# Kernel optimization log

Hardware: AMD Instinct MI355X
Metric: run time of the kernel (lower is better)

The kernel has to match this reference:

```python
import jax, jax.numpy as jnp
import numpy as np

B, TQ, TK, D, DV = 16, 2048, 2048, 128, 128
MASK_VAL = -1000000.0

def setup_inputs() -> dict:
    key = jax.random.key(0)
    kq, kk, kv, kl = jax.random.split(key, 4)
    q = jax.random.normal(kq, (B, TQ, D), dtype=jnp.float32)
    k = jax.random.normal(kk, (B, TK, D), dtype=jnp.float32)
    v = jax.random.normal(kv, (B, TK, DV), dtype=jnp.float32)
    valid_lens = jax.random.randint(kl, (B,), 1, TK, dtype=jnp.int64)
    return {"q": q, "k": k, "v": v, "valid_lens": valid_lens}

def reference(q, k, v, valid_lens):
    d = q.shape[-1]
    # scores: [B, Tq, Tk]
    scores = jnp.einsum('bqd,bkd->bqk', q, k) / jnp.sqrt(jnp.asarray(d, q.dtype))
    # mask key positions >= valid_len (same per-batch length for every query row)
    mask = jnp.arange(scores.shape[-1])[None, None, :] < valid_lens[:, None, None]
    scores = jnp.where(mask, scores, jnp.asarray(MASK_VAL, scores.dtype))
    attn = jax.nn.softmax(scores, axis=-1)
    # dropout p=0.0 (eval mode) -> identity
    return jnp.einsum('bqk,bkv->bqv', attn, v)
```

## Files before the change

kernel.cpp:

```cpp
#include <hip/hip_runtime.h>
#include <math.h>

#define NB 16
#define TQ 2048
#define TK 2048
#define DD 128
#define DVV 128

constexpr int QTILE = 64;
constexpr int KTILE = 32;
#define PSTR 40

typedef __attribute__((ext_vector_type(8))) _Float16 half8;
typedef __attribute__((ext_vector_type(4))) _Float16 half4;
typedef __attribute__((ext_vector_type(4))) float f32x4;

__device__ inline float fast_exp2(float x) {
#if __has_builtin(__builtin_amdgcn_exp2f)
    return __builtin_amdgcn_exp2f(x);
#else
    return exp2f(x);
#endif
}
__device__ inline void setprio1() { __builtin_amdgcn_s_setprio(1); }
__device__ inline void setprio0() { __builtin_amdgcn_s_setprio(0); }

__device__ inline void glds16(const _Float16* g, _Float16* l) {
    __builtin_amdgcn_global_load_lds(
        (const __attribute__((address_space(1))) void*)g,
        (__attribute__((address_space(3))) void*)l, 16, 0, 0);
}

__global__ __launch_bounds__(256)
void repack(const float* __restrict__ kg, const float* __restrict__ vg,
            const int* __restrict__ vlg,
            _Float16* __restrict__ Kpk, _Float16* __restrict__ Vpk)
{
    const int bt = blockIdx.x;
    const int b = bt >> 6, t = bt & 63;
    if (t * KTILE >= vlg[b]) return;
    const int tid = threadIdx.x;

    __shared__ float Vlds[32][129];

    const float* kin = kg + ((size_t)b * TK + t * KTILE) * DD;
    _Float16* kout = Kpk + ((size_t)bt << 12);
#pragma unroll
    for (int pp = 0; pp < 2; ++pp) {
        int s = tid + pp * 256;
        int ct = s >> 8, c = (s >> 6) & 3, ln = s & 63;
        int kr = ct * 16 + (ln & 15), kc = c * 32 + ((ln >> 4) & 3) * 8;
        const float* ip = kin + kr * DD + kc;
        float4 f0 = *(const float4*)ip;
        float4 f1 = *(const float4*)(ip + 4);
        half8 h;
        h[0] = (_Float16)f0.x; h[1] = (_Float16)f0.y;
        h[2] = (_Float16)f0.z; h[3] = (_Float16)f0.w;
        h[4] = (_Float16)f1.x; h[5] = (_Float16)f1.y;
        h[6] = (_Float16)f1.z; h[7] = (_Float16)f1.w;
        *(half8*)(kout + (size_t)s * 8) = h;
    }

    const float* vin = vg + ((size_t)b * TK + t * KTILE) * DVV;
#pragma unroll
    for (int pp = 0; pp < 4; ++pp) {
        int idx = tid + pp * 256;
        int r = idx >> 5, c4 = (idx & 31) * 4;
        float4 f = *(const float4*)(vin + r * DVV + c4);
        Vlds[r][c4 + 0] = f.x; Vlds[r][c4 + 1] = f.y;
        Vlds[r][c4 + 2] = f.z; Vlds[r][c4 + 3] = f.w;
    }
    __syncthreads();
    _Float16* vout = Vpk + ((size_t)bt << 12);
#pragma unroll
    for (int pp = 0; pp < 2; ++pp) {
        int s = tid + pp * 256;
        int n = s >> 6, ln = s & 63;
        int dv = n * 16 + (ln & 15), k0 = ((ln >> 4) & 3) * 8;
        half8 h;
#pragma unroll
        for (int j = 0; j < 8; ++j)
            h[j] = (_Float16)Vlds[k0 + j][dv];
        *(half8*)(vout + (size_t)s * 8) = h;
    }
}

__global__ __launch_bounds__(256, 4)
void attn_fwd(const float* __restrict__ qg,
              const _Float16* __restrict__ Kpk, const _Float16* __restrict__ Vpk,
              const int* __restrict__ vlg,
              float* __restrict__ outg, float* __restrict__ wso,
              float* __restrict__ wsml, int ns)
{
    __shared__ _Float16 Kb[2][4096];
    __shared__ _Float16 Vb[2][4096];
    __shared__ _Float16 Plds[4][16][PSTR];

    const int tid  = threadIdx.x;
    const int wid  = tid >> 6;
    const int lane = tid & 63;
    const int l15  = lane & 15;
    const int lhi  = lane >> 4;

    const int bid   = blockIdx.x;
    const int b     = bid & (NB - 1);
    const int qbase = (bid >> 4) * QTILE;
    const int sp    = blockIdx.y;

    const int VL  = vlg[b];
    const int nkt = (VL + KTILE - 1) / KTILE;
    const int tps = (nkt + ns - 1) / ns;
    const int t0  = sp * tps;
    const int t1  = min(nkt, t0 + tps);
    if (t0 >= t1) return;

    const _Float16* ktb = Kpk + ((size_t)(b * 64) << 12);
    const _Float16* vtb = Vpk + ((size_t)(b * 64) << 12);

    half8 qf[4];
    {
        const float scale = 0.08838834764831845f * 1.4426950408889634f;
        const int qrow = qbase + wid * 16 + l15;
        const float* qp = qg + (size_t)(b * TQ + qrow) * DD + lhi * 8;
#pragma unroll
        for (int c = 0; c < 4; ++c) {
            float4 f0 = *(const float4*)(qp + c * 32);
            float4 f1 = *(const float4*)(qp + c * 32 + 4);
            half8 t;
            t[0] = (_Float16)(f0.x * scale); t[1] = (_Float16)(f0.y * scale);
            t[2] = (_Float16)(f0.z * scale); t[3] = (_Float16)(f0.w * scale);
            t[4] = (_Float16)(f1.x * scale); t[5] = (_Float16)(f1.y * scale);
            t[6] = (_Float16)(f1.z * scale); t[7] = (_Float16)(f1.w * scale);
            qf[c] = t;
        }
    }

    auto STAGE = [&](int buf, int t) {
        const _Float16* kp = ktb + ((size_t)t << 12) + wid * 1024 + lane * 8;
        const _Float16* vp = vtb + ((size_t)t << 12) + wid * 1024 + lane * 8;
        glds16(kp,       &Kb[buf][wid * 1024]);
        glds16(kp + 512, &Kb[buf][wid * 1024 + 512]);
        glds16(vp,       &Vb[buf][wid * 1024]);
        glds16(vp + 512, &Vb[buf][wid * 1024 + 512]);
    };

    float m_i = -INFINITY, l_i = 0.f;
    f32x4 o[8];
#pragma unroll
    for (int n = 0; n < 8; ++n) { f32x4 z = {0.f, 0.f, 0.f, 0.f}; o[n] = z; }

    STAGE(0, t0);
    int cur = 0;
    for (int t = t0; t < t1; ++t) {
        const int kb = t * KTILE;
        const bool pre = (t + 1 < t1);
        if (pre) STAGE(cur ^ 1, t + 1);

        if (pre) asm volatile("s_waitcnt vmcnt(4)\ns_barrier" ::: "memory");
        else     asm volatile("s_waitcnt vmcnt(0)\ns_barrier" ::: "memory");

        const half8* kp = (const half8*)&Kb[cur][0];
        const half8* vp = (const half8*)&Vb[cur][0];

        f32x4 sc[2];
        setprio1();
#pragma unroll
        for (int ct = 0; ct < 2; ++ct) {
            f32x4 z = {0.f, 0.f, 0.f, 0.f};
            sc[ct] = z;
#pragma unroll
            for (int c = 0; c < 4; ++c) {
                half8 kf = kp[ct * 256 + c * 64 + lane];
                sc[ct] = __builtin_amdgcn_mfma_f32_16x16x32_f16(kf, qf[c], sc[ct], 0, 0, 0);
            }
        }
        setprio0();

        if (kb + KTILE > VL) {
#pragma unroll
            for (int ct = 0; ct < 2; ++ct) {
                const int kg = kb + ct * 16 + lhi * 4;
#pragma unroll
                for (int r = 0; r < 4; ++r)
                    if (kg + r >= VL) sc[ct][r] = -1e30f;
            }
        }

        float mx = sc[0][0];
#pragma unroll
        for (int ct = 0; ct < 2; ++ct)
#pragma unroll
            for (int r = 0; r < 4; ++r) mx = fmaxf(mx, sc[ct][r]);
        mx = fmaxf(mx, __shfl_xor(mx, 16));
        mx = fmaxf(mx, __shfl_xor(mx, 32));

        const bool skip = __all(mx <= m_i + 8.0f);
        const float mnew = skip ? m_i : fmaxf(m_i, mx);

        float p[8];
        float sum = 0.f;
#pragma unroll
        for (int ct = 0; ct < 2; ++ct)
#pragma unroll
            for (int r = 0; r < 4; ++r) {
                float e = fast_exp2(sc[ct][r] - mnew);
                p[ct * 4 + r] = e;
                sum += e;
            }
        sum += __shfl_xor(sum, 16);
        sum += __shfl_xor(sum, 32);

#pragma unroll
        for (int ct = 0; ct < 2; ++ct) {
            half4 ph;
            ph[0] = (_Float16)p[ct * 4 + 0]; ph[1] = (_Float16)p[ct * 4 + 1];
            ph[2] = (_Float16)p[ct * 4 + 2]; ph[3] = (_Float16)p[ct * 4 + 3];
            *(half4*)&Plds[wid][l15][ct * 16 + lhi * 4] = ph;
        }

        if (skip) {
            l_i += sum;
        } else {
            const float corr = fast_exp2(m_i - mnew);
            l_i = l_i * corr + sum;
            m_i = mnew;
            float cr[4];
#pragma unroll
            for (int r = 0; r < 4; ++r)
                cr[r] = __shfl(corr, (lane & 48) | (lhi * 4 + r));
#pragma unroll
            for (int n = 0; n < 8; ++n)
#pragma unroll
                for (int r = 0; r < 4; ++r) o[n][r] *= cr[r];
        }

        half8 pa = *(const half8*)&Plds[wid][l15][lhi * 8];
        setprio1();
#pragma unroll
        for (int n = 0; n < 8; ++n) {
            half8 vb = vp[n * 64 + lane];
            o[n] = __builtin_amdgcn_mfma_f32_16x16x32_f16(pa, vb, o[n], 0, 0, 0);
        }
        setprio0();

        asm volatile("s_waitcnt lgkmcnt(0)\ns_barrier" ::: "memory");
        cur ^= 1;
    }

    if (ns == 1) {
        float li4[4];
#pragma unroll
        for (int r = 0; r < 4; ++r) {
            float lr = __shfl(l_i, (lane & 48) | (lhi * 4 + r));
            li4[r] = 1.0f / lr;
        }
#pragma unroll
        for (int r = 0; r < 4; ++r) {
            const int qrow = qbase + wid * 16 + lhi * 4 + r;
            float* op = outg + (size_t)(b * TQ + qrow) * DVV + l15;
#pragma unroll
            for (int n = 0; n < 8; ++n)
                op[n * 16] = o[n][r] * li4[r];
        }
    } else {
        if (lhi == 0) {
            float2 ml = make_float2(m_i, l_i);
            *(float2*)&wsml[((size_t)(sp * NB + b) * TQ + qbase + wid * 16 + l15) * 2] = ml;
        }
        float* po = wso + ((size_t)(sp * NB + b) * TQ + qbase + wid * 16) * DVV;
#pragma unroll
        for (int r = 0; r < 4; ++r)
#pragma unroll
            for (int n = 0; n < 8; ++n)
                po[(lhi * 4 + r) * DVV + n * 16 + l15] = o[n][r];
    }
}

__global__ __launch_bounds__(256)
void attn_combine(const float* __restrict__ wso, const float* __restrict__ wsml,
                  const int* __restrict__ vlg, float* __restrict__ outg, int ns)
{
    const int idx = blockIdx.x * 256 + threadIdx.x;
    const int d4 = idx & 31;
    const int q  = (idx >> 5) & (TQ - 1);
    const int b  = idx >> 16;

    const int VL  = vlg[b];
    const int nkt = (VL + KTILE - 1) / KTILE;
    const int tps = (nkt + ns - 1) / ns;
    const int nv  = (nkt + tps - 1) / tps;

    float M = -1e30f, den = 0.f;
    f32x4 acc = {0.f, 0.f, 0.f, 0.f};
    for (int s = 0; s < nv; ++s) {
        const size_t row = (size_t)(s * NB + b) * TQ + q;
        float2 ml = *(const float2*)&wsml[row * 2];
        float Mn = fmaxf(M, ml.x);
        float c  = fast_exp2(M - Mn);
        float w  = fast_exp2(ml.x - Mn);
        f32x4 ov = *(const f32x4*)&wso[row * DVV + d4 * 4];
        acc = acc * c + ov * w;
        den = den * c + w * ml.y;
        M = Mn;
    }
    const float inv = 1.0f / den;
    f32x4 r = acc * inv;
    *(f32x4*)&outg[((size_t)b * TQ + q) * DVV + d4 * 4] = r;
}

extern "C" void kernel_launch(void* const* d_in, const int* in_sizes, int n_in,
                              void* d_out, int out_size, void* d_ws, size_t ws_size,
                              hipStream_t stream) {
    const float* q  = (const float*)d_in[0];
    const float* k  = (const float*)d_in[1];
    const float* v  = (const float*)d_in[2];
    const int*   vl = (const int*)d_in[3];
    float* out = (float*)d_out;

    const size_t pk_elems = (size_t)NB * 64 * 4096;
    const size_t pk_bytes = pk_elems * sizeof(_Float16);
    const size_t o_elems  = (size_t)NB * TQ * DVV;
    const size_t ml_elems = (size_t)NB * TQ * 2;
    const size_t per_split = (o_elems + ml_elems) * sizeof(float);

    int ns = (ws_size >= 2 * pk_bytes + 2 * per_split) ? 2 : 1;

    _Float16* Kpk = (_Float16*)d_ws;
    _Float16* Vpk = Kpk + pk_elems;
    float* wso  = (float*)(Vpk + pk_elems);
    float* wsml = wso + (size_t)ns * o_elems;

    hipLaunchKernelGGL(repack, dim3(NB * 64), dim3(256), 0, stream,
                       k, v, vl, Kpk, Vpk);

    dim3 grid(NB * (TQ / QTILE), ns);
    hipLaunchKernelGGL(attn_fwd, grid, dim3(256), 0, stream,
                       q, Kpk, Vpk, vl, out, wso, wsml, ns);

    if (ns > 1) {
        dim3 cgrid((NB * TQ * (DVV / 4)) / 256);
        hipLaunchKernelGGL(attn_combine, cgrid, dim3(256), 0, stream,
                           wso, wsml, vl, out, ns);
    }
}
```

Measured before the change: 73.04 us.

## Use 128-row Q tiles with 8 waves, fp16 split partials, and up to 4 splits

Doubles the query tile to 128 rows and the block to 512 threads (8 waves), so each staged K/V tile feeds twice as many queries. Each wave now issues half as many async loads, with waves 0-3 loading K and 4-7 loading V. Split-K partial outputs are stored in fp16 instead of fp32, which halves workspace traffic. The split count can rise to 4 when the workspace allows. The fp16 partials lose some accuracy, and more splits add combine work.

```diff
diff --git a/kernel.cpp b/kernel.cpp
--- a/kernel.cpp
+++ b/kernel.cpp
@@ -7,7 +7,7 @@
 #define DD 128
 #define DVV 128
 
-constexpr int QTILE = 64;
+constexpr int QTILE = 128;
 constexpr int KTILE = 32;
 #define PSTR 40
 
@@ -85,16 +85,16 @@
     }
 }
 
-__global__ __launch_bounds__(256, 4)
+__global__ __launch_bounds__(512, 6)
 void attn_fwd(const float* __restrict__ qg,
               const _Float16* __restrict__ Kpk, const _Float16* __restrict__ Vpk,
               const int* __restrict__ vlg,
-              float* __restrict__ outg, float* __restrict__ wso,
+              float* __restrict__ outg, _Float16* __restrict__ wso,
               float* __restrict__ wsml, int ns)
 {
     __shared__ _Float16 Kb[2][4096];
     __shared__ _Float16 Vb[2][4096];
-    __shared__ _Float16 Plds[4][16][PSTR];
+    __shared__ _Float16 Plds[8][16][PSTR];
 
     const int tid  = threadIdx.x;
     const int wid  = tid >> 6;
@@ -135,13 +135,13 @@
         }
     }
 
+    const int qtr = wid & 3;
     auto STAGE = [&](int buf, int t) {
-        const _Float16* kp = ktb + ((size_t)t << 12) + wid * 1024 + lane * 8;
-        const _Float16* vp = vtb + ((size_t)t << 12) + wid * 1024 + lane * 8;
-        glds16(kp,       &Kb[buf][wid * 1024]);
-        glds16(kp + 512, &Kb[buf][wid * 1024 + 512]);
-        glds16(vp,       &Vb[buf][wid * 1024]);
-        glds16(vp + 512, &Vb[buf][wid * 1024 + 512]);
+        const _Float16* src = ((wid < 4) ? ktb : vtb)
+                              + ((size_t)t << 12) + qtr * 1024 + lane * 8;
+        _Float16* dst = (wid < 4) ? &Kb[buf][qtr * 1024] : &Vb[buf][qtr * 1024];
+        glds16(src, dst);
+        glds16(src + 512, dst + 512);
     };
 
     float m_i = -INFINITY, l_i = 0.f;
@@ -156,7 +156,7 @@
         const bool pre = (t + 1 < t1);
         if (pre) STAGE(cur ^ 1, t + 1);
 
-        if (pre) asm volatile("s_waitcnt vmcnt(4)\ns_barrier" ::: "memory");
+        if (pre) asm volatile("s_waitcnt vmcnt(2)\ns_barrier" ::: "memory");
         else     asm volatile("s_waitcnt vmcnt(0)\ns_barrier" ::: "memory");
 
         const half8* kp = (const half8*)&Kb[cur][0];
@@ -267,23 +267,23 @@
             float2 ml = make_float2(m_i, l_i);
             *(float2*)&wsml[((size_t)(sp * NB + b) * TQ + qbase + wid * 16 + l15) * 2] = ml;
         }
-        float* po = wso + ((size_t)(sp * NB + b) * TQ + qbase + wid * 16) * DVV;
+        _Float16* po = wso + ((size_t)(sp * NB + b) * TQ + qbase + wid * 16) * DVV;
 #pragma unroll
         for (int r = 0; r < 4; ++r)
 #pragma unroll
             for (int n = 0; n < 8; ++n)
-                po[(lhi * 4 + r) * DVV + n * 16 + l15] = o[n][r];
+                po[(lhi * 4 + r) * DVV + n * 16 + l15] = (_Float16)o[n][r];
     }
 }
 
 __global__ __launch_bounds__(256)
-void attn_combine(const float* __restrict__ wso, const float* __restrict__ wsml,
+void attn_combine(const _Float16* __restrict__ wso, const float* __restrict__ wsml,
                   const int* __restrict__ vlg, float* __restrict__ outg, int ns)
 {
     const int idx = blockIdx.x * 256 + threadIdx.x;
-    const int d4 = idx & 31;
-    const int q  = (idx >> 5) & (TQ - 1);
-    const int b  = idx >> 16;
+    const int d8 = idx & 15;
+    const int q  = (idx >> 4) & (TQ - 1);
+    const int b  = idx >> 15;
 
     const int VL  = vlg[b];
     const int nkt = (VL + KTILE - 1) / KTILE;
@@ -291,21 +291,26 @@
     const int nv  = (nkt + tps - 1) / tps;
 
     float M = -1e30f, den = 0.f;
-    f32x4 acc = {0.f, 0.f, 0.f, 0.f};
+    float acc[8] = {0.f, 0.f, 0.f, 0.f, 0.f, 0.f, 0.f, 0.f};
     for (int s = 0; s < nv; ++s) {
         const size_t row = (size_t)(s * NB + b) * TQ + q;
         float2 ml = *(const float2*)&wsml[row * 2];
         float Mn = fmaxf(M, ml.x);
         float c  = fast_exp2(M - Mn);
         float w  = fast_exp2(ml.x - Mn);
-        f32x4 ov = *(const f32x4*)&wso[row * DVV + d4 * 4];
-        acc = acc * c + ov * w;
+        half8 ov = *(const half8*)&wso[row * DVV + d8 * 8];
+#pragma unroll
+        for (int j = 0; j < 8; ++j)
+            acc[j] = acc[j] * c + (float)ov[j] * w;
         den = den * c + w * ml.y;
         M = Mn;
     }
     const float inv = 1.0f / den;
-    f32x4 r = acc * inv;
-    *(f32x4*)&outg[((size_t)b * TQ + q) * DVV + d4 * 4] = r;
+    float* op = outg + ((size_t)b * TQ + q) * DVV + d8 * 8;
+    f32x4 r0 = {acc[0] * inv, acc[1] * inv, acc[2] * inv, acc[3] * inv};
+    f32x4 r1 = {acc[4] * inv, acc[5] * inv, acc[6] * inv, acc[7] * inv};
+    *(f32x4*)op = r0;
+    *(f32x4*)(op + 4) = r1;
 }
 
 extern "C" void kernel_launch(void* const* d_in, const int* in_sizes, int n_in,
@@ -318,27 +323,29 @@
     float* out = (float*)d_out;
 
     const size_t pk_elems = (size_t)NB * 64 * 4096;
-    const size_t pk_bytes = pk_elems * sizeof(_Float16);
+    const size_t pk_bytes = 2 * pk_elems * sizeof(_Float16);
     const size_t o_elems  = (size_t)NB * TQ * DVV;
     const size_t ml_elems = (size_t)NB * TQ * 2;
-    const size_t per_split = (o_elems + ml_elems) * sizeof(float);
-
-    int ns = (ws_size >= 2 * pk_bytes + 2 * per_split) ? 2 : 1;
+    const size_t per_split = o_elems * sizeof(_Float16) + ml_elems * sizeof(float);
+
+    int ns = 1;
+    if (ws_size >= pk_bytes + 4 * per_split) ns = 4;
+    else if (ws_size >= pk_bytes + 2 * per_split) ns = 2;
 
     _Float16* Kpk = (_Float16*)d_ws;
     _Float16* Vpk = Kpk + pk_elems;
-    float* wso  = (float*)(Vpk + pk_elems);
-    float* wsml = wso + (size_t)ns * o_elems;
+    _Float16* wso  = Vpk + pk_elems;
+    float*    wsml = (float*)(wso + (size_t)ns * o_elems);
 
     hipLaunchKernelGGL(repack, dim3(NB * 64), dim3(256), 0, stream,
                        k, v, vl, Kpk, Vpk);
 
     dim3 grid(NB * (TQ / QTILE), ns);
-    hipLaunchKernelGGL(attn_fwd, grid, dim3(256), 0, stream,
+    hipLaunchKernelGGL(attn_fwd, grid, dim3(512), 0, stream,
                        q, Kpk, Vpk, vl, out, wso, wsml, ns);
 
     if (ns > 1) {
-        dim3 cgrid((NB * TQ * (DVV / 4)) / 256);
+        dim3 cgrid((NB * TQ * 16) / 256);
         hipLaunchKernelGGL(attn_combine, cgrid, dim3(256), 0, stream,
                            wso, wsml, vl, out, ns);
     }
```

Result: no change. 71.71 us (-1.8%).
